# Kernel tuning notes

Hardware: AMD Instinct MI355X
Metric: run time of the kernel (lower is better)

The kernel has to match this reference:

```python
import jax, jax.numpy as jnp
import numpy as np

N = 50000      # nodes
E = 400000     # directed edges (self-loops added inside reference, per PyG default)
DIN = 256
DH = 32
HEADS = 8
DOUT = 40
SLOPE = 0.2    # GATv2Conv negative_slope default


def _gatv2_layer(x, src, dst, Wl, bl, Wr, br, att, bias, heads, out_ch):
    """One GATv2Conv (concat=True). x:[n,din], src/dst:[e], att:[heads,out_ch]."""
    n = x.shape[0]
    xl = (x @ Wl + bl).reshape(n, heads, out_ch)   # source transform
    xr = (x @ Wr + br).reshape(n, heads, out_ch)   # target transform
    e = jax.nn.leaky_relu(xl[src] + xr[dst], SLOPE)          # [e, H, C]
    s = jnp.einsum('ehc,hc->eh', e, att)                     # per-edge attention logits
    smax = jax.ops.segment_max(s, dst, num_segments=n)       # stable softmax over in-edges
    ex = jnp.exp(s - smax[dst])
    denom = jax.ops.segment_sum(ex, dst, num_segments=n)
    alpha = ex / denom[dst]                                  # [e, H]
    out = jax.ops.segment_sum(alpha[:, :, None] * xl[src], dst, num_segments=n)
    return out.reshape(n, heads * out_ch) + bias


def setup_inputs() -> dict:
    key = jax.random.key(0)
    ks = jax.random.split(key, 8)
    def gl(k, shape, fan_in):
        return jax.random.normal(k, shape, jnp.float32) * np.float32(1.0 / np.sqrt(fan_in))
    return {
        'x': jax.random.normal(ks[0], (N, DIN), jnp.float32),
        'edge_index': jax.random.randint(ks[1], (2, E), 0, N, jnp.int32),
        'W1l': gl(ks[2], (DIN, HEADS * DH), DIN),
        'b1l': jnp.zeros((HEADS * DH,), jnp.float32),
        'W1r': gl(ks[3], (DIN, HEADS * DH), DIN),
        'b1r': jnp.zeros((HEADS * DH,), jnp.float32),
        'att1': gl(ks[4], (HEADS, DH), DH),
        'bias1': jnp.zeros((HEADS * DH,), jnp.float32),
        'W2l': gl(ks[5], (HEADS * DH, DOUT), HEADS * DH),
        'b2l': jnp.zeros((DOUT,), jnp.float32),
        'W2r': gl(ks[6], (HEADS * DH, DOUT), HEADS * DH),
        'b2r': jnp.zeros((DOUT,), jnp.float32),
        'att2': gl(ks[7], (1, DOUT), DOUT),
        'bias2': jnp.zeros((DOUT,), jnp.float32),
    }


def reference(x, edge_index, W1l, b1l, W1r, b1r, att1, bias1,
              W2l, b2l, W2r, b2r, att2, bias2):
    n = x.shape[0]
    loop = jnp.arange(n, dtype=edge_index.dtype)  # add_self_loops=True (PyG default)
    src = jnp.concatenate([edge_index[0], loop])
    dst = jnp.concatenate([edge_index[1], loop])
    # eval mode: F.dropout is identity; normalization='none' -> Identity
    h = _gatv2_layer(x, src, dst, W1l, b1l, W1r, b1r, att1, bias1, HEADS, DH)
    h = jax.nn.elu(h)
    out = _gatv2_layer(h, src, dst, W2l, b2l, W2r, b2r, att2, bias2, 1, DOUT)
    return jax.nn.log_softmax(out, axis=1)
```

## Files before the change

kernel.cpp:

```cpp
#include <hip/hip_runtime.h>
#include <math.h>

#define NODES 50000
#define NEDGE 400000
#define ETOT  450000
#define DIN   256
#define C1    256
#define C2    40
#define CPAD  64
#define CSRCAP (NODES * CPAD)
#define NB_CNT ((ETOT + 255) / 256)
#define NB_CVT (NODES * DIN / 8 / 256)

typedef __attribute__((ext_vector_type(8))) short bfrag;
typedef __attribute__((ext_vector_type(4))) float facc;

#define GPTR(p) (const __attribute__((address_space(1))) unsigned int*)(p)
#define LPTR(p) (__attribute__((address_space(3))) unsigned int*)(p)

static __device__ __forceinline__ float bitsf(unsigned int x) {
    float f;
    __builtin_memcpy(&f, &x, 4);
    return f;
}
static __device__ __forceinline__ unsigned short f2bf(float f) {
    unsigned int x;
    __builtin_memcpy(&x, &f, 4);
    unsigned int r = x + 0x7fffu + ((x >> 16) & 1u);
    return (unsigned short)(r >> 16);
}
static __device__ __forceinline__ float fexp2(float x) {
#if __has_builtin(__builtin_amdgcn_exp2f)
    return __builtin_amdgcn_exp2f(x);
#else
    return exp2f(x);
#endif
}

__global__ __launch_bounds__(256)
void prep_a(const int* __restrict__ srcRow, const int* __restrict__ dstRow,
            int* __restrict__ cnt, int* __restrict__ csr,
            const float* __restrict__ x, unsigned short* __restrict__ xb)
{
    if (blockIdx.x < NB_CNT) {
        int e = blockIdx.x * 256 + threadIdx.x;
        if (e >= ETOT) return;
        int d, s;
        if (e < NEDGE) { d = dstRow[e]; s = srcRow[e]; }
        else           { d = e - NEDGE; s = d; }
        int slot = atomicAdd(&cnt[d], 1);
        csr[(d << 6) + slot] = s;
    } else {
        int i = (blockIdx.x - NB_CNT) * 256 + threadIdx.x;
        const float4* p = (const float4*)x + (size_t)i * 2;
        float4 u0 = p[0], u1 = p[1];
        bfrag pk;
        pk[0] = (short)f2bf(u0.x); pk[1] = (short)f2bf(u0.y);
        pk[2] = (short)f2bf(u0.z); pk[3] = (short)f2bf(u0.w);
        pk[4] = (short)f2bf(u1.x); pk[5] = (short)f2bf(u1.y);
        pk[6] = (short)f2bf(u1.z); pk[7] = (short)f2bf(u1.w);
        *(bfrag*)(xb + (size_t)i * 8) = pk;
    }
}

__global__ __launch_bounds__(256)
void prep_ww(const float* __restrict__ W1l, const float* __restrict__ W1r,
             unsigned short* __restrict__ Wt1,
             const float* __restrict__ W2l, const float* __restrict__ W2r,
             unsigned short* __restrict__ Wt2)
{
    if (blockIdx.x < 512) {
        const int idx = blockIdx.x * 256 + threadIdx.x;
        const int n = idx >> 8;
        const int k = idx & 255;
        float v = (n < C1) ? W1l[(size_t)k * C1 + n] : W1r[(size_t)k * C1 + (n - C1)];
        Wt1[idx] = f2bf(v);
    } else {
        const int idx = (blockIdx.x - 512) * 256 + threadIdx.x;
        const int n = idx >> 8;
        const int k = idx & 255;
        if (n >= 2 * C2) return;
        float v = (n < C2) ? W2l[(size_t)k * C2 + n] : W2r[(size_t)k * C2 + (n - C2)];
        Wt2[idx] = f2bf(v);
    }
}

#define GBM 128
#define GBN 128
#define GBK 32

template<typename OUTT, bool SWZ>
__global__ __launch_bounds__(256)
void mfma_gemm(const unsigned short* __restrict__ Ab, const unsigned short* __restrict__ Bt,
               const float* __restrict__ bl, const float* __restrict__ br,
               OUTT* __restrict__ Cl, OUTT* __restrict__ Cr,
               int M, int Nrows, int Nhalf, int nbnShift)
{
    __shared__ __align__(16) unsigned short As[3][GBM * GBK];
    __shared__ __align__(16) unsigned short Bs[3][GBN * GBK];

    const int tid  = threadIdx.x;
    const int lane = tid & 63;
    const int w    = tid >> 6;
    const int wr   = w >> 1;
    const int wc   = w & 1;

    int tile;
    if constexpr (SWZ) {
        const int nwg = gridDim.x;
        const int q = nwg >> 3, r = nwg & 7;
        const int xcd = blockIdx.x & 7;
        const int idx = blockIdx.x >> 3;
        tile = (xcd < r ? xcd * (q + 1) : r * (q + 1) + (xcd - r) * q) + idx;
    } else {
        tile = blockIdx.x;
    }
    const int bx   = tile >> nbnShift;
    const int by   = tile & ((1 << nbnShift) - 1);
    const int row0 = bx * GBM;
    const int col0 = by * GBN;

    facc acc[4][4];
    #pragma unroll
    for (int i = 0; i < 4; ++i)
        #pragma unroll
        for (int j = 0; j < 4; ++j) {
            facc z = {0.f, 0.f, 0.f, 0.f};
            acc[i][j] = z;
        }

    const int rA  = lane >> 2;
    const int kgA = (lane & 3) ^ ((rA >> 1) & 3);
    const int fr    = lane & 15;
    const int sRead = (lane >> 4) ^ ((fr >> 1) & 3);

    #define STAGE(bufi, k0)                                                     \
    {                                                                           \
        _Pragma("unroll")                                                       \
        for (int p = 0; p < 2; ++p) {                                           \
            const int chunk = p * 4 + w;                                        \
            const int r_loc = chunk * 16 + rA;                                  \
            const int ga = min(row0 + r_loc, M - 1);                            \
            __builtin_amdgcn_global_load_lds(                                   \
                GPTR(Ab + (size_t)ga * 256 + (k0) + kgA * 8),                   \
                LPTR(&As[bufi][chunk * 512]), 16, 0, 0);                        \
            const int gb = min(col0 + r_loc, Nrows - 1);                        \
            __builtin_amdgcn_global_load_lds(                                   \
                GPTR(Bt + (size_t)gb * 256 + (k0) + kgA * 8),                   \
                LPTR(&Bs[bufi][chunk * 512]), 16, 0, 0);                        \
        }                                                                       \
    }

    #define KSTEP(T, WSTR)                                                      \
    {                                                                           \
        asm volatile("s_waitcnt vmcnt(" WSTR ")" ::: "memory");                 \
        __builtin_amdgcn_s_barrier();                                           \
        __builtin_amdgcn_sched_barrier(0);                                      \
        constexpr int cur = (T) % 3;                                            \
        bfrag af[4], bfv[4];                                                    \
        _Pragma("unroll")                                                       \
        for (int mi = 0; mi < 4; ++mi)                                          \
            af[mi] = *(const bfrag*)(&As[cur][(wr * 64 + mi * 16 + fr) * 32 + sRead * 8]); \
        _Pragma("unroll")                                                       \
        for (int ni = 0; ni < 4; ++ni)                                          \
            bfv[ni] = *(const bfrag*)(&Bs[cur][(wc * 64 + ni * 16 + fr) * 32 + sRead * 8]); \
        if constexpr ((T) + 2 < 8) STAGE(((T) + 2) % 3, ((T) + 2) * GBK);       \
        _Pragma("unroll")                                                       \
        for (int mi = 0; mi < 4; ++mi)                                          \
            _Pragma("unroll")                                                   \
            for (int ni = 0; ni < 4; ++ni)                                      \
                acc[mi][ni] = __builtin_amdgcn_mfma_f32_16x16x32_bf16(          \
                    af[mi], bfv[ni], acc[mi][ni], 0, 0, 0);                     \
    }

    STAGE(0, 0 * GBK);
    STAGE(1, 1 * GBK);
    KSTEP(0, "4"); KSTEP(1, "4"); KSTEP(2, "4"); KSTEP(3, "4");
    KSTEP(4, "4"); KSTEP(5, "4"); KSTEP(6, "4"); KSTEP(7, "0");
    #undef KSTEP
    #undef STAGE

    #pragma unroll
    for (int mi = 0; mi < 4; ++mi) {
        const int rbase = row0 + wr * 64 + mi * 16 + ((lane >> 4) << 2);
        #pragma unroll
        for (int ni = 0; ni < 4; ++ni) {
            const int col = col0 + wc * 64 + ni * 16 + (lane & 15);
            #pragma unroll
            for (int rg = 0; rg < 4; ++rg) {
                int r = rbase + rg;
                if (r >= M) continue;
                float v = acc[mi][ni][rg];
                if (col < Nhalf) {
                    v += bl[col];
                    if constexpr (sizeof(OUTT) == 2)
                        Cl[(size_t)r * Nhalf + col] = (OUTT)f2bf(v);
                    else
                        Cl[(size_t)r * Nhalf + col] = (OUTT)v;
                } else if (col < 2 * Nhalf) {
                    int c2 = col - Nhalf;
                    v += br[c2];
                    if constexpr (sizeof(OUTT) == 2)
                        Cr[(size_t)r * Nhalf + c2] = (OUTT)f2bf(v);
                    else
                        Cr[(size_t)r * Nhalf + c2] = (OUTT)v;
                }
            }
        }
    }
}

__global__ __launch_bounds__(256)
void fused_l1(const int* __restrict__ deg,
              const int* __restrict__ csr, const unsigned short* __restrict__ xl,
              const unsigned short* __restrict__ xr, const float* __restrict__ att,
              const float* __restrict__ bias, unsigned short* __restrict__ hout)
{
    const int lane = threadIdx.x & 63;
    const int n    = blockIdx.x * 4 + (threadIdx.x >> 6);
    if (n >= NODES) return;

    const int a  = n << 6;
    const int dn = __builtin_amdgcn_readfirstlane(deg[n]);
    const int np = (dn + 3) & ~3;

    const uint2 xrn = *(const uint2*)(xr + (size_t)n * C1 + lane * 4);
    const float xr0 = bitsf(xrn.x << 16), xr1 = bitsf(xrn.x & 0xffff0000u);
    const float xr2 = bitsf(xrn.y << 16), xr3 = bitsf(xrn.y & 0xffff0000u);
    const float4 wv = *(const float4*)(att + lane * 4);
    const float L2E = 1.4426950408889634f;
    const float w6_0 = wv.x * (0.6f * L2E), w4_0 = wv.x * (0.4f * L2E);
    const float w6_1 = wv.y * (0.6f * L2E), w4_1 = wv.y * (0.4f * L2E);
    const float w6_2 = wv.z * (0.6f * L2E), w4_2 = wv.z * (0.4f * L2E);
    const float w6_3 = wv.w * (0.6f * L2E), w4_3 = wv.w * (0.4f * L2E);

    float m = -INFINITY, d = 0.f;
    float a0 = 0.f, a1 = 0.f, a2 = 0.f, a3 = 0.f;

    uint2 R[4];
    {
        const int4 s4 = *(const int4*)(csr + a);
        R[0] = *(const uint2*)(xl + (size_t)s4.x * C1 + lane * 4);
        R[1] = *(const uint2*)(xl + (size_t)s4.y * C1 + lane * 4);
        R[2] = *(const uint2*)(xl + (size_t)s4.z * C1 + lane * 4);
        R[3] = *(const uint2*)(xl + (size_t)s4.w * C1 + lane * 4);
    }

    for (int i = 0; i < np; i += 4) {
        uint2 Rn[4];
        const int nx = (i + 4 < np) ? (i + 4) : i;
        {
            const int4 s4 = *(const int4*)(csr + a + nx);
            Rn[0] = *(const uint2*)(xl + (size_t)s4.x * C1 + lane * 4);
            Rn[1] = *(const uint2*)(xl + (size_t)s4.y * C1 + lane * 4);
            Rn[2] = *(const uint2*)(xl + (size_t)s4.z * C1 + lane * 4);
            Rn[3] = *(const uint2*)(xl + (size_t)s4.w * C1 + lane * 4);
        }

        float x0[4], x1[4], x2[4], x3[4], p[4];
        #pragma unroll
        for (int k = 0; k < 4; ++k) {
            x0[k] = bitsf(R[k].x << 16);
            x1[k] = bitsf(R[k].x & 0xffff0000u);
            x2[k] = bitsf(R[k].y << 16);
            x3[k] = bitsf(R[k].y & 0xffff0000u);
            const float v0 = x0[k] + xr0, v1 = x1[k] + xr1;
            const float v2 = x2[k] + xr2, v3 = x3[k] + xr3;
            float pp;
            pp = w6_0 * v0;
            pp = fmaf(w4_0, fabsf(v0), pp);
            pp = fmaf(w6_1, v1, pp);
            pp = fmaf(w4_1, fabsf(v1), pp);
            pp = fmaf(w6_2, v2, pp);
            pp = fmaf(w4_2, fabsf(v2), pp);
            pp = fmaf(w6_3, v3, pp);
            pp = fmaf(w4_3, fabsf(v3), pp);
            pp += __shfl_xor(pp, 1);
            pp += __shfl_xor(pp, 2);
            pp += __shfl_xor(pp, 4);
            p[k] = (i + k < dn) ? pp : -INFINITY;
        }

        const float pm = fmaxf(fmaxf(p[0], p[1]), fmaxf(p[2], p[3]));
        if (__any(pm > m + 8.f)) {
            #pragma unroll
            for (int k = 0; k < 4; ++k) {
                const float mN = fmaxf(m, p[k]);
                const float sc = fexp2(m - mN);
                const float wg = fexp2(p[k] - mN);
                m = mN;
                d = fmaf(d, sc, wg);
                a0 = fmaf(wg, x0[k], a0 * sc);
                a1 = fmaf(wg, x1[k], a1 * sc);
                a2 = fmaf(wg, x2[k], a2 * sc);
                a3 = fmaf(wg, x3[k], a3 * sc);
            }
        } else {
            #pragma unroll
            for (int k = 0; k < 4; ++k) {
                const float wg = fexp2(p[k] - m);
                d += wg;
                a0 = fmaf(wg, x0[k], a0);
                a1 = fmaf(wg, x1[k], a1);
                a2 = fmaf(wg, x2[k], a2);
                a3 = fmaf(wg, x3[k], a3);
            }
        }

        #pragma unroll
        for (int k = 0; k < 4; ++k) R[k] = Rn[k];
    }

    const float inv = 1.f / d;
    const float4 bv = *(const float4*)(bias + lane * 4);
    float v0 = fmaf(a0, inv, bv.x), v1 = fmaf(a1, inv, bv.y);
    float v2 = fmaf(a2, inv, bv.z), v3 = fmaf(a3, inv, bv.w);
    v0 = v0 > 0.f ? v0 : (fexp2(v0 * L2E) - 1.f);
    v1 = v1 > 0.f ? v1 : (fexp2(v1 * L2E) - 1.f);
    v2 = v2 > 0.f ? v2 : (fexp2(v2 * L2E) - 1.f);
    v3 = v3 > 0.f ? v3 : (fexp2(v3 * L2E) - 1.f);
    uint2 o;
    o.x = (unsigned int)f2bf(v0) | ((unsigned int)f2bf(v1) << 16);
    o.y = (unsigned int)f2bf(v2) | ((unsigned int)f2bf(v3) << 16);
    *(uint2*)(hout + (size_t)n * C1 + lane * 4) = o;
}

__global__ __launch_bounds__(256)
void fused_l2(const int* __restrict__ deg,
              const int* __restrict__ csr, const float* __restrict__ h2l,
              const float* __restrict__ h2r, const float* __restrict__ att,
              const float* __restrict__ bias, float* __restrict__ out)
{
    const int lane = threadIdx.x & 63;
    const int n    = blockIdx.x * 4 + (threadIdx.x >> 6);
    if (n >= NODES) return;
    const int l8 = lane & 7;
    const int g  = lane >> 3;

    const int a  = n << 6;
    const int dn = __builtin_amdgcn_readfirstlane(deg[n]);
    const float L2E = 1.4426950408889634f;

    float w6[5], w4[5], xr[5];
    #pragma unroll
    for (int j = 0; j < 5; ++j) {
        const int c = l8 + 8 * j;
        const float w = att[c];
        w6[j] = w * (0.6f * L2E);
        w4[j] = w * (0.4f * L2E);
        xr[j] = h2r[(size_t)n * C2 + c];
    }

    float m = -INFINITY, dl = 0.f;
    float acc[5] = {0.f, 0.f, 0.f, 0.f, 0.f};

    float R[5];
    {
        const int src = csr[a + g];
        const float* row = h2l + (size_t)src * C2 + l8;
        #pragma unroll
        for (int j = 0; j < 5; ++j) R[j] = row[8 * j];
    }

    for (int c0 = 0; c0 < dn; c0 += 8) {
        float Rn[5];
        {
            const int nx = (c0 + 8 < dn) ? (c0 + 8) : c0;
            const int src = csr[a + nx + g];
            const float* row = h2l + (size_t)src * C2 + l8;
            #pragma unroll
            for (int j = 0; j < 5; ++j) Rn[j] = row[8 * j];
        }

        const int idx = c0 + g;
        float p = 0.f;
        #pragma unroll
        for (int j = 0; j < 5; ++j) {
            const float v = R[j] + xr[j];
            p = fmaf(w6[j], v, p);
            p = fmaf(w4[j], fabsf(v), p);
        }
        p += __shfl_xor(p, 1);
        p += __shfl_xor(p, 2);
        p += __shfl_xor(p, 4);
        if (idx >= dn) p = -INFINITY;

        if (__any(p > m + 8.f)) {
            float pm = p;
            pm = fmaxf(pm, __shfl_xor(pm, 8));
            pm = fmaxf(pm, __shfl_xor(pm, 16));
            pm = fmaxf(pm, __shfl_xor(pm, 32));
            const float mN = fmaxf(m, pm);
            const float sc = fexp2(m - mN);
            const float wg = fexp2(p - mN);
            m = mN;
            dl = fmaf(dl, sc, wg);
            #pragma unroll
            for (int j = 0; j < 5; ++j) acc[j] = fmaf(wg, R[j], acc[j] * sc);
        } else {
            const float wg = fexp2(p - m);
            dl += wg;
            #pragma unroll
            for (int j = 0; j < 5; ++j) acc[j] = fmaf(wg, R[j], acc[j]);
        }

        #pragma unroll
        for (int j = 0; j < 5; ++j) R[j] = Rn[j];
    }

    #pragma unroll
    for (int o = 8; o < 64; o <<= 1) {
        dl += __shfl_xor(dl, o);
        #pragma unroll
        for (int j = 0; j < 5; ++j) acc[j] += __shfl_xor(acc[j], o);
    }

    const float inv = 1.f / dl;
    float v[5];
    float mx = -INFINITY;
    #pragma unroll
    for (int j = 0; j < 5; ++j) {
        v[j] = fmaf(acc[j], inv, bias[l8 + 8 * j]);
        mx = fmaxf(mx, v[j]);
    }
    mx = fmaxf(mx, __shfl_xor(mx, 1));
    mx = fmaxf(mx, __shfl_xor(mx, 2));
    mx = fmaxf(mx, __shfl_xor(mx, 4));
    float s = 0.f;
    #pragma unroll
    for (int j = 0; j < 5; ++j) s += fexp2((v[j] - mx) * L2E);
    s += __shfl_xor(s, 1);
    s += __shfl_xor(s, 2);
    s += __shfl_xor(s, 4);
    const float lg = logf(s);
    if (g == 0) {
        #pragma unroll
        for (int j = 0; j < 5; ++j)
            out[(size_t)n * C2 + l8 + 8 * j] = v[j] - mx - lg;
    }
}

extern "C" void kernel_launch(void* const* d_in, const int* in_sizes, int n_in,
                              void* d_out, int out_size, void* d_ws, size_t ws_size,
                              hipStream_t stream)
{
    const float* x     = (const float*)d_in[0];
    const int*   ei    = (const int*)  d_in[1];
    const float* W1l   = (const float*)d_in[2];
    const float* b1l   = (const float*)d_in[3];
    const float* W1r   = (const float*)d_in[4];
    const float* b1r   = (const float*)d_in[5];
    const float* att1  = (const float*)d_in[6];
    const float* bias1 = (const float*)d_in[7];
    const float* W2l   = (const float*)d_in[8];
    const float* b2l   = (const float*)d_in[9];
    const float* W2r   = (const float*)d_in[10];
    const float* b2r   = (const float*)d_in[11];
    const float* att2  = (const float*)d_in[12];
    const float* bias2 = (const float*)d_in[13];
    float* out = (float*)d_out;

    float* ws = (float*)d_ws;
    unsigned short* xl1 = (unsigned short*)ws;
    unsigned short* xr1 = (unsigned short*)(ws + 6400000);
    unsigned short* xb  = (unsigned short*)(ws + 12800000);
    int*   csr    = (int*)(ws + 19200000);
    int*   cnt    = csr + CSRCAP;
    unsigned short* Wt1 = (unsigned short*)(ws + 22500000);
    unsigned short* Wt2 = (unsigned short*)(ws + 22600000);
    unsigned short* h = xr1;
    float* h2l = ws;
    float* h2r = ws + 2000000;

    const int* srcRow = ei;
    const int* dstRow = ei + NEDGE;

    hipMemsetAsync(cnt, 0, NODES * sizeof(int), stream);
    hipMemsetAsync(csr, 0, CSRCAP * sizeof(int), stream);
    prep_a<<<NB_CNT + NB_CVT, 256, 0, stream>>>(srcRow, dstRow, cnt, csr, x, xb);
    prep_ww<<<512 + 80, 256, 0, stream>>>(W1l, W1r, Wt1, W2l, W2r, Wt2);

    mfma_gemm<unsigned short, true><<<((NODES + GBM - 1) / GBM) * 4, 256, 0, stream>>>(
        xb, Wt1, b1l, b1r, xl1, xr1, NODES, 2 * C1, C1, 2);
    fused_l1<<<(NODES + 3) / 4, 256, 0, stream>>>(cnt, csr, xl1, xr1, att1, bias1, h);

    mfma_gemm<float, false><<<(NODES + GBM - 1) / GBM, 256, 0, stream>>>(
        h, Wt2, b2l, b2r, h2l, h2r, NODES, 2 * C2, C2, 0);
    fused_l2<<<(NODES + 3) / 4, 256, 0, stream>>>(cnt, csr, h2l, h2r, att2, bias2, out);
}
```

Before: 184.3 us.

## Replace layer-1 GEMM with single-wave 64x64 tile kernel without block barriers

Adds a new layer-1 GEMM kernel that uses one 64-thread wavefront per 64x64 output tile, with double-buffered direct global-to-LDS loads synchronized only by vmcnt waits. Because a single wave owns each tile, no __syncthreads are needed. The grid is 8 column blocks by 782 row blocks, which gives many small blocks so more of them can be resident at once. The trade-off is less data reuse per tile and more redundant A/B loads than the 128x128, 256-thread kernel. The output stores are scalar bf16 writes with per-element bias adds.

Measured after the change: 195.0 us. 5.8% more time.

```diff
diff --git a/kernel.cpp b/kernel.cpp
--- a/kernel.cpp
+++ b/kernel.cpp
@@ -82,6 +82,102 @@
         if (n >= 2 * C2) return;
         float v = (n < C2) ? W2l[(size_t)k * C2 + n] : W2r[(size_t)k * C2 + (n - C2)];
         Wt2[idx] = f2bf(v);
+    }
+}
+
+__global__ __launch_bounds__(64)
+void gemm1_nb(const unsigned short* __restrict__ Ab, const unsigned short* __restrict__ Bt,
+              const float* __restrict__ bl, const float* __restrict__ br,
+              unsigned short* __restrict__ Cl, unsigned short* __restrict__ Cr,
+              int M, int Nhalf)
+{
+    __shared__ __align__(16) unsigned short As[2][64 * 32];
+    __shared__ __align__(16) unsigned short Bs[2][64 * 32];
+
+    const int lane = threadIdx.x;
+    const int cb = blockIdx.x / 784;
+    const int p  = blockIdx.x - cb * 784;
+    if (p >= 782) return;
+    const int row0 = p * 64;
+    const int col0 = cb * 64;
+
+    facc acc[4][4];
+    #pragma unroll
+    for (int i = 0; i < 4; ++i)
+        #pragma unroll
+        for (int j = 0; j < 4; ++j) {
+            facc z = {0.f, 0.f, 0.f, 0.f};
+            acc[i][j] = z;
+        }
+
+    const int rA  = lane >> 2;
+    const int kgA = (lane & 3) ^ ((rA >> 1) & 3);
+    const int fr    = lane & 15;
+    const int sRead = (lane >> 4) ^ ((fr >> 1) & 3);
+
+    #define STAGE(bufi, k0)                                                     \
+    {                                                                           \
+        _Pragma("unroll")                                                       \
+        for (int c = 0; c < 4; ++c) {                                           \
+            const int ga = min(row0 + c * 16 + rA, M - 1);                      \
+            __builtin_amdgcn_global_load_lds(                                   \
+                GPTR(Ab + (size_t)ga * 256 + (k0) + kgA * 8),                   \
+                LPTR(&As[bufi][c * 512]), 16, 0, 0);                            \
+            const int gb = col0 + c * 16 + rA;                                  \
+            __builtin_amdgcn_global_load_lds(                                   \
+                GPTR(Bt + (size_t)gb * 256 + (k0) + kgA * 8),                   \
+                LPTR(&Bs[bufi][c * 512]), 16, 0, 0);                            \
+        }                                                                       \
+    }
+
+    #define KSTEP(T, WSTR)                                                      \
+    {                                                                           \
+        asm volatile("s_waitcnt vmcnt(" WSTR ")" ::: "memory");                 \
+        constexpr int cur = (T) & 1;                                            \
+        bfrag af[4], bfv[4];                                                    \
+        _Pragma("unroll")                                                       \
+        for (int mi = 0; mi < 4; ++mi)                                          \
+            af[mi] = *(const bfrag*)(&As[cur][(mi * 16 + fr) * 32 + sRead * 8]); \
+        _Pragma("unroll")                                                       \
+        for (int ni = 0; ni < 4; ++ni)                                          \
+            bfv[ni] = *(const bfrag*)(&Bs[cur][(ni * 16 + fr) * 32 + sRead * 8]); \
+        if constexpr ((T) + 2 < 8) STAGE(((T) + 2) & 1, ((T) + 2) * 32);        \
+        _Pragma("unroll")                                                       \
+        for (int mi = 0; mi < 4; ++mi)                                          \
+            _Pragma("unroll")                                                   \
+            for (int ni = 0; ni < 4; ++ni)                                      \
+                acc[mi][ni] = __builtin_amdgcn_mfma_f32_16x16x32_bf16(          \
+                    af[mi], bfv[ni], acc[mi][ni], 0, 0, 0);                     \
+    }
+
+    STAGE(0, 0);
+    STAGE(1, 32);
+    KSTEP(0, "8"); KSTEP(1, "8"); KSTEP(2, "8"); KSTEP(3, "8");
+    KSTEP(4, "8"); KSTEP(5, "8"); KSTEP(6, "8"); KSTEP(7, "0");
+    #undef KSTEP
+    #undef STAGE
+
+    #pragma unroll
+    for (int mi = 0; mi < 4; ++mi) {
+        const int rbase = row0 + mi * 16 + ((lane >> 4) << 2);
+        #pragma unroll
+        for (int ni = 0; ni < 4; ++ni) {
+            const int col = col0 + ni * 16 + fr;
+            #pragma unroll
+            for (int rg = 0; rg < 4; ++rg) {
+                const int rr = rbase + rg;
+                if (rr >= M) continue;
+                float v = acc[mi][ni][rg];
+                if (col < Nhalf) {
+                    v += bl[col];
+                    Cl[(size_t)rr * Nhalf + col] = f2bf(v);
+                } else {
+                    const int c2 = col - Nhalf;
+                    v += br[c2];
+                    Cr[(size_t)rr * Nhalf + c2] = f2bf(v);
+                }
+            }
+        }
     }
 }
 
@@ -480,8 +576,7 @@
     prep_a<<<NB_CNT + NB_CVT, 256, 0, stream>>>(srcRow, dstRow, cnt, csr, x, xb);
     prep_ww<<<512 + 80, 256, 0, stream>>>(W1l, W1r, Wt1, W2l, W2r, Wt2);
 
-    mfma_gemm<unsigned short, true><<<((NODES + GBM - 1) / GBM) * 4, 256, 0, stream>>>(
-        xb, Wt1, b1l, b1r, xl1, xr1, NODES, 2 * C1, C1, 2);
+    gemm1_nb<<<784 * 8, 64, 0, stream>>>(xb, Wt1, b1l, b1r, xl1, xr1, NODES, C1);
     fused_l1<<<(NODES + 3) / 4, 256, 0, stream>>>(cnt, csr, xl1, xr1, att1, bias1, h);
 
     mfma_gemm<float, false><<<(NODES + GBM - 1) / GBM, 256, 0, stream>>>(
```

## Split layer-1 aggregation wave into two half-waves with 16-byte feature loads

Applied to the files above, without the earlier changes.

Layer-1 aggregation is restructured so each 64-lane wave splits into two 32-lane halves. Each half handles alternate edge pairs, with every lane covering 8 channels through uint4 loads instead of 4 channels through uint2. The two halves keep separate online-softmax states and merge them at the end with a cross-half shuffle. This widens the gather loads and shortens the attention-logit shuffle reduction, at the cost of more registers per lane and an extra merge step.

Measured after the change: 182.2 us (median of 2 runs). About the same (-1.1%).

```diff
diff --git a/kernel.cpp b/kernel.cpp
--- a/kernel.cpp
+++ b/kernel.cpp
@@ -219,110 +219,145 @@
     const int lane = threadIdx.x & 63;
     const int n    = blockIdx.x * 4 + (threadIdx.x >> 6);
     if (n >= NODES) return;
+    const int eh  = lane >> 5;
+    const int l32 = lane & 31;
+    const int c0  = l32 * 8;
 
     const int a  = n << 6;
     const int dn = __builtin_amdgcn_readfirstlane(deg[n]);
     const int np = (dn + 3) & ~3;
 
-    const uint2 xrn = *(const uint2*)(xr + (size_t)n * C1 + lane * 4);
-    const float xr0 = bitsf(xrn.x << 16), xr1 = bitsf(xrn.x & 0xffff0000u);
-    const float xr2 = bitsf(xrn.y << 16), xr3 = bitsf(xrn.y & 0xffff0000u);
-    const float4 wv = *(const float4*)(att + lane * 4);
     const float L2E = 1.4426950408889634f;
-    const float w6_0 = wv.x * (0.6f * L2E), w4_0 = wv.x * (0.4f * L2E);
-    const float w6_1 = wv.y * (0.6f * L2E), w4_1 = wv.y * (0.4f * L2E);
-    const float w6_2 = wv.z * (0.6f * L2E), w4_2 = wv.z * (0.4f * L2E);
-    const float w6_3 = wv.w * (0.6f * L2E), w4_3 = wv.w * (0.4f * L2E);
-
-    float m = -INFINITY, d = 0.f;
-    float a0 = 0.f, a1 = 0.f, a2 = 0.f, a3 = 0.f;
-
-    uint2 R[4];
+    const float MINIT = -1e30f, MMASK = -2e30f;
+
+    float xrv[8];
     {
-        const int4 s4 = *(const int4*)(csr + a);
-        R[0] = *(const uint2*)(xl + (size_t)s4.x * C1 + lane * 4);
-        R[1] = *(const uint2*)(xl + (size_t)s4.y * C1 + lane * 4);
-        R[2] = *(const uint2*)(xl + (size_t)s4.z * C1 + lane * 4);
-        R[3] = *(const uint2*)(xl + (size_t)s4.w * C1 + lane * 4);
-    }
+        const uint4 u = *(const uint4*)(xr + (size_t)n * C1 + c0);
+        xrv[0] = bitsf(u.x << 16); xrv[1] = bitsf(u.x & 0xffff0000u);
+        xrv[2] = bitsf(u.y << 16); xrv[3] = bitsf(u.y & 0xffff0000u);
+        xrv[4] = bitsf(u.z << 16); xrv[5] = bitsf(u.z & 0xffff0000u);
+        xrv[6] = bitsf(u.w << 16); xrv[7] = bitsf(u.w & 0xffff0000u);
+    }
+    float w6[8], w4[8];
+    {
+        const float4 wa = *(const float4*)(att + c0);
+        const float4 wb = *(const float4*)(att + c0 + 4);
+        const float wv[8] = {wa.x, wa.y, wa.z, wa.w, wb.x, wb.y, wb.z, wb.w};
+        #pragma unroll
+        for (int j = 0; j < 8; ++j) {
+            w6[j] = wv[j] * (0.6f * L2E);
+            w4[j] = wv[j] * (0.4f * L2E);
+        }
+    }
+
+    float m = MINIT, d = 0.f;
+    float acc[8] = {0.f, 0.f, 0.f, 0.f, 0.f, 0.f, 0.f, 0.f};
+
+    #define LOADG(D0, D1, I)                                                     \
+    {                                                                            \
+        const int2 s2 = *(const int2*)(csr + a + (I) + 2 * eh);                  \
+        D0 = *(const uint4*)(xl + (size_t)s2.x * C1 + c0);                       \
+        D1 = *(const uint4*)(xl + (size_t)s2.y * C1 + c0);                       \
+    }
+    #define UNPACK(X, U)                                                         \
+        X[0] = bitsf(U.x << 16); X[1] = bitsf(U.x & 0xffff0000u);                \
+        X[2] = bitsf(U.y << 16); X[3] = bitsf(U.y & 0xffff0000u);                \
+        X[4] = bitsf(U.z << 16); X[5] = bitsf(U.z & 0xffff0000u);                \
+        X[6] = bitsf(U.w << 16); X[7] = bitsf(U.w & 0xffff0000u);
+
+    uint4 R0, R1;
+    LOADG(R0, R1, 0);
 
     for (int i = 0; i < np; i += 4) {
-        uint2 Rn[4];
-        const int nx = (i + 4 < np) ? (i + 4) : i;
-        {
-            const int4 s4 = *(const int4*)(csr + a + nx);
-            Rn[0] = *(const uint2*)(xl + (size_t)s4.x * C1 + lane * 4);
-            Rn[1] = *(const uint2*)(xl + (size_t)s4.y * C1 + lane * 4);
-            Rn[2] = *(const uint2*)(xl + (size_t)s4.z * C1 + lane * 4);
-            Rn[3] = *(const uint2*)(xl + (size_t)s4.w * C1 + lane * 4);
-        }
-
-        float x0[4], x1[4], x2[4], x3[4], p[4];
-        #pragma unroll
-        for (int k = 0; k < 4; ++k) {
-            x0[k] = bitsf(R[k].x << 16);
-            x1[k] = bitsf(R[k].x & 0xffff0000u);
-            x2[k] = bitsf(R[k].y << 16);
-            x3[k] = bitsf(R[k].y & 0xffff0000u);
-            const float v0 = x0[k] + xr0, v1 = x1[k] + xr1;
-            const float v2 = x2[k] + xr2, v3 = x3[k] + xr3;
-            float pp;
-            pp = w6_0 * v0;
-            pp = fmaf(w4_0, fabsf(v0), pp);
-            pp = fmaf(w6_1, v1, pp);
-            pp = fmaf(w4_1, fabsf(v1), pp);
-            pp = fmaf(w6_2, v2, pp);
-            pp = fmaf(w4_2, fabsf(v2), pp);
-            pp = fmaf(w6_3, v3, pp);
-            pp = fmaf(w4_3, fabsf(v3), pp);
-            pp += __shfl_xor(pp, 1);
-            pp += __shfl_xor(pp, 2);
-            pp += __shfl_xor(pp, 4);
-            p[k] = (i + k < dn) ? pp : -INFINITY;
-        }
-
-        const float pm = fmaxf(fmaxf(p[0], p[1]), fmaxf(p[2], p[3]));
+        uint4 Rn0, Rn1;
+        LOADG(Rn0, Rn1, i + 4);
+
+        float x0[8], x1[8];
+        UNPACK(x0, R0)
+        UNPACK(x1, R1)
+
+        float p0 = 0.f, p1 = 0.f;
+        #pragma unroll
+        for (int j = 0; j < 8; ++j) {
+            const float v = x0[j] + xrv[j];
+            p0 = fmaf(w6[j], v, p0);
+            p0 = fmaf(w4[j], fabsf(v), p0);
+        }
+        #pragma unroll
+        for (int j = 0; j < 8; ++j) {
+            const float v = x1[j] + xrv[j];
+            p1 = fmaf(w6[j], v, p1);
+            p1 = fmaf(w4[j], fabsf(v), p1);
+        }
+        p0 += __shfl_xor(p0, 1); p0 += __shfl_xor(p0, 2);
+        p1 += __shfl_xor(p1, 1); p1 += __shfl_xor(p1, 2);
+        const int e0 = i + 2 * eh;
+        p0 = (e0     < dn) ? p0 : MMASK;
+        p1 = (e0 + 1 < dn) ? p1 : MMASK;
+
+        const float pm = fmaxf(p0, p1);
         if (__any(pm > m + 8.f)) {
-            #pragma unroll
-            for (int k = 0; k < 4; ++k) {
-                const float mN = fmaxf(m, p[k]);
-                const float sc = fexp2(m - mN);
-                const float wg = fexp2(p[k] - mN);
-                m = mN;
-                d = fmaf(d, sc, wg);
-                a0 = fmaf(wg, x0[k], a0 * sc);
-                a1 = fmaf(wg, x1[k], a1 * sc);
-                a2 = fmaf(wg, x2[k], a2 * sc);
-                a3 = fmaf(wg, x3[k], a3 * sc);
-            }
+            float mN = fmaxf(m, p0);
+            float sc = fexp2(m - mN);
+            float wg = fexp2(p0 - mN);
+            m = mN;
+            d = fmaf(d, sc, wg);
+            #pragma unroll
+            for (int j = 0; j < 8; ++j) acc[j] = fmaf(wg, x0[j], acc[j] * sc);
+            mN = fmaxf(m, p1);
+            sc = fexp2(m - mN);
+            wg = fexp2(p1 - mN);
+            m = mN;
+            d = fmaf(d, sc, wg);
+            #pragma unroll
+            for (int j = 0; j < 8; ++j) acc[j] = fmaf(wg, x1[j], acc[j] * sc);
         } else {
-            #pragma unroll
-            for (int k = 0; k < 4; ++k) {
-                const float wg = fexp2(p[k] - m);
-                d += wg;
-                a0 = fmaf(wg, x0[k], a0);
-                a1 = fmaf(wg, x1[k], a1);
-                a2 = fmaf(wg, x2[k], a2);
-                a3 = fmaf(wg, x3[k], a3);
-            }
-        }
-
-        #pragma unroll
-        for (int k = 0; k < 4; ++k) R[k] = Rn[k];
+            const float wg0 = fexp2(p0 - m);
+            const float wg1 = fexp2(p1 - m);
+            d += wg0 + wg1;
+            #pragma unroll
+            for (int j = 0; j < 8; ++j)
+                acc[j] = fmaf(wg1, x1[j], fmaf(wg0, x0[j], acc[j]));
+        }
+
+        R0 = Rn0; R1 = Rn1;
+    }
+    #undef LOADG
+    #undef UNPACK
+
+    {
+        const float mo = __shfl_xor(m, 32);
+        const float mN = fmaxf(m, mo);
+        const float sc = fexp2(m - mN);
+        d *= sc;
+        d += __shfl_xor(d, 32);
+        #pragma unroll
+        for (int j = 0; j < 8; ++j) {
+            acc[j] *= sc;
+            acc[j] += __shfl_xor(acc[j], 32);
+        }
     }
 
     const float inv = 1.f / d;
-    const float4 bv = *(const float4*)(bias + lane * 4);
-    float v0 = fmaf(a0, inv, bv.x), v1 = fmaf(a1, inv, bv.y);
-    float v2 = fmaf(a2, inv, bv.z), v3 = fmaf(a3, inv, bv.w);
-    v0 = v0 > 0.f ? v0 : (fexp2(v0 * L2E) - 1.f);
-    v1 = v1 > 0.f ? v1 : (fexp2(v1 * L2E) - 1.f);
-    v2 = v2 > 0.f ? v2 : (fexp2(v2 * L2E) - 1.f);
-    v3 = v3 > 0.f ? v3 : (fexp2(v3 * L2E) - 1.f);
-    uint2 o;
-    o.x = (unsigned int)f2bf(v0) | ((unsigned int)f2bf(v1) << 16);
-    o.y = (unsigned int)f2bf(v2) | ((unsigned int)f2bf(v3) << 16);
-    *(uint2*)(hout + (size_t)n * C1 + lane * 4) = o;
+    float vv[8];
+    {
+        const float4 ba = *(const float4*)(bias + c0);
+        const float4 bb = *(const float4*)(bias + c0 + 4);
+        const float bv[8] = {ba.x, ba.y, ba.z, ba.w, bb.x, bb.y, bb.z, bb.w};
+        #pragma unroll
+        for (int j = 0; j < 8; ++j) {
+            float v = fmaf(acc[j], inv, bv[j]);
+            vv[j] = v > 0.f ? v : (fexp2(v * L2E) - 1.f);
+        }
+    }
+    if (eh == 0) {
+        uint4 o;
+        o.x = (unsigned int)f2bf(vv[0]) | ((unsigned int)f2bf(vv[1]) << 16);
+        o.y = (unsigned int)f2bf(vv[2]) | ((unsigned int)f2bf(vv[3]) << 16);
+        o.z = (unsigned int)f2bf(vv[4]) | ((unsigned int)f2bf(vv[5]) << 16);
+        o.w = (unsigned int)f2bf(vv[6]) | ((unsigned int)f2bf(vv[7]) << 16);
+        *(uint4*)(hout + (size_t)n * C1 + c0) = o;
+    }
 }
 
 __global__ __launch_bounds__(256)
```
